# Performance work log

Hardware: AMD Instinct MI355X
Metric: run time of the kernel (lower is better)

Reference implementation:

```python
import jax, jax.numpy as jnp
import numpy as np


def setup_inputs() -> dict:
    key = jax.random.key(0)
    ks = jax.random.split(key, 15)
    B, r, d, h, na = 64, 64, 2048, 64, 256
    x = jax.random.normal(ks[0], (B, d, na), dtype=jnp.float32)
    L = jax.random.randint(ks[1], (B, 2, na), 0, 2).astype(jnp.float32)
    p = lambda i, shp: jax.random.normal(ks[i], shp, dtype=jnp.float32)
    return {
        "x": x, "L": L,
        "Aq": p(2, (r, d)), "Ak": p(3, (r, d)), "Av": p(4, (r, d)),
        "Aq1": p(5, (r, r)), "Ak1": p(6, (r, r)), "Av1": p(7, (r, r)),
        "Aq5": p(8, (r, r)), "Ak5": p(9, (r, r)), "Av5": p(10, (r, r)),
        "Ao": p(11, (r, r)), "Ao1": p(12, (r, r)), "Ao5": p(13, (h, r)),
    }


def reference(x, L, Aq, Ak, Av, Aq1, Ak1, Av1, Aq5, Ak5, Av5, Ao, Ao1, Ao5):
    B, d, na = x.shape
    # numNeighbors: count of L[:,0,:] >= 1 per batch, +1 -> [B,1,1]
    numN = jnp.sum((L[:, 0, :] >= 1.0).astype(jnp.float32), axis=1)[:, None, None] + 1.0
    scale = jnp.sqrt(numN)  # [B,1,1]

    def attn(M, Wq, Wk, Wv):
        # M: [B, f, na]; Wq/Wk/Wv: [r, f]
        Q = jax.nn.sigmoid(jnp.einsum('rf,bfn->bnr', Wq, M))  # [B,na,r]
        K = jax.nn.sigmoid(jnp.einsum('rf,bfn->brn', Wk, M))  # [B,r,na]
        V = jax.nn.sigmoid(jnp.einsum('rf,bfn->bnr', Wv, M))  # [B,na,r]
        A = jax.nn.softmax(jnp.einsum('bnr,brm->bnm', Q, K) / scale, axis=2)
        return jnp.einsum('bnm,bmr->brn', A, V)  # [B,r,na]

    o = attn(x, Aq, Ak, Av)
    M = jax.nn.silu(jnp.einsum('sr,brn->bsn', Ao, o))
    o = attn(M, Aq1, Ak1, Av1)
    M = jax.nn.silu(jnp.einsum('sr,brn->bsn', Ao1, o))
    o = attn(M, Aq5, Ak5, Av5)
    M = jax.nn.silu(jnp.einsum('hr,brn->bhn', Ao5, o))  # [B,h,na]

    blk = d // na  # rows per block (8)
    def diagvec(i):
        # kron(sum-of-squares, ones(1,2)) == repeat each element twice -> [B, 2*na]
        return jnp.repeat(jnp.sum(M[:, i * blk:(i + 1) * blk, :] ** 2, axis=1), 2, axis=1)

    M11, M12, M21, M22 = diagvec(0), diagvec(1), diagvec(2), diagvec(3)
    Mpp = jnp.sum(M[:, 4 * blk:, :] ** 2, axis=1)  # [B, na]

    # q = x[:, :4, :].transpose(1,2).reshape(B, 4*na) (agent-major ordering)
    q = jnp.transpose(x[:, :4, :], (0, 2, 1)).reshape(B, 4 * na)
    q1, q2 = q[:, :2 * na], q[:, 2 * na:]
    # Block matrix [[diag(M11), diag(M12)], [diag(M21), diag(M22)]] quadratic form,
    # computed without materializing the [B, 4na, 4na] matrix.
    quad = jnp.sum(M11 * q1 * q1 + M12 * q1 * q2 + M21 * q2 * q1 + M22 * q2 * q2,
                   axis=1, keepdims=True)
    return quad + jnp.sum(Mpp, axis=1, keepdims=True)  # [B, 1]
```

## Files before the change

### kernel.cpp

```cpp
#include <hip/hip_runtime.h>
#include <stdint.h>

typedef _Float16 f16;
typedef f16 f16x8 __attribute__((ext_vector_type(8)));
typedef float f32x4 __attribute__((ext_vector_type(4)));

#define MFMA(a,b,c) __builtin_amdgcn_mfma_f32_16x16x32_f16(a, b, c, 0, 0, 0)

__device__ __forceinline__ float sigmoidf_(float z) {
  return __builtin_amdgcn_rcpf(1.0f + __expf(-z));
}

__global__ void prep_kernel(const float* __restrict__ L,
    const float* __restrict__ Aq, const float* __restrict__ Ak, const float* __restrict__ Av,
    const float* __restrict__ Aq1, const float* __restrict__ Ak1, const float* __restrict__ Av1,
    const float* __restrict__ Aq5, const float* __restrict__ Ak5, const float* __restrict__ Av5,
    const float* __restrict__ Ao, const float* __restrict__ Ao1, const float* __restrict__ Ao5,
    float* __restrict__ scale, f16* __restrict__ Wcat, f16* __restrict__ Wsm,
    float* __restrict__ out)
{
  __shared__ float r4[4];
  int blk = blockIdx.x, t = threadIdx.x;
  if (blk < 64) {
    float v = (L[blk * 512 + t] >= 1.0f) ? 1.0f : 0.0f;
    #pragma unroll
    for (int off = 32; off; off >>= 1) v += __shfl_down(v, off);
    if ((t & 63) == 0) r4[t >> 6] = v;
    __syncthreads();
    if (t == 0) scale[blk] = sqrtf(r4[0] + r4[1] + r4[2] + r4[3] + 1.0f);
  } else if (blk < 160) {
    int base = (blk - 64) * 4096;
    for (int i = 0; i < 16; i++) {
      int idx = base + t + i * 256;
      int row = idx >> 11, col = idx & 2047;
      float v = (row < 64) ? Aq[row * 2048 + col]
              : (row < 128) ? Ak[(row - 64) * 2048 + col]
              : Av[(row - 128) * 2048 + col];
      Wcat[idx] = (f16)v;
    }
  } else if (blk < 169) {
    int j = blk - 160;
    const float* s = (j == 0) ? Aq1 : (j == 1) ? Ak1 : (j == 2) ? Av1 : (j == 3) ? Aq5
                   : (j == 4) ? Ak5 : (j == 5) ? Av5 : (j == 6) ? Ao : (j == 7) ? Ao1 : Ao5;
    for (int i = 0; i < 16; i++) { int idx = t + i * 256; Wsm[j * 4096 + idx] = (f16)s[idx]; }
  } else {
    if (t < 64) out[t] = 0.0f;
  }
}

__global__ __launch_bounds__(256) void qkv1_kernel(const float* __restrict__ x,
    const f16* __restrict__ Wcat, f16* __restrict__ Qt, f16* __restrict__ Kt,
    f16* __restrict__ Vg)
{
  int b = blockIdx.y, n0 = blockIdx.x * 32;
  int t = threadIdx.x, lane = t & 63, w = t >> 6;
  int l15 = lane & 15, q = lane >> 4;
  __shared__ f16 xt[2][32 * 76];
  __shared__ f16 wt[2][192 * 76];
  f32x4 acc[2][3] = {};
  const float* xb = x + (size_t)b * 524288 + n0;
  int tn = t & 31, fg = t >> 5;

  int r0 = t >> 3,           c0 = t & 7;
  int r1 = (t + 256) >> 3,   c1 = (t + 256) & 7;
  int r2 = (t + 512) >> 3,   c2 = (t + 512) & 7;
  int r3 = (t + 768) >> 3,   c3 = (t + 768) & 7;
  int r4 = (t + 1024) >> 3,  c4 = (t + 1024) & 7;
  int r5 = (t + 1280) >> 3,  c5 = (t + 1280) & 7;
  const f16* pw0 = Wcat + (size_t)r0 * 2048 + c0 * 8;
  const f16* pw1 = Wcat + (size_t)r1 * 2048 + c1 * 8;
  const f16* pw2 = Wcat + (size_t)r2 * 2048 + c2 * 8;
  const f16* pw3 = Wcat + (size_t)r3 * 2048 + c3 * 8;
  const f16* pw4 = Wcat + (size_t)r4 * 2048 + c4 * 8;
  const f16* pw5 = Wcat + (size_t)r5 * 2048 + c5 * 8;
  const float* px = xb + (size_t)(fg * 8) * 256 + tn;

  float xa0, xa1, xa2, xa3, xa4, xa5, xa6, xa7;
  uint4 wr0, wr1, wr2, wr3, wr4, wr5;

#define LOAD_X(f0n) do {                                                        \
    const float* xp_ = px + (size_t)(f0n) * 256;                                \
    xa0 = xp_[0];    xa1 = xp_[256];  xa2 = xp_[512];  xa3 = xp_[768];          \
    xa4 = xp_[1024]; xa5 = xp_[1280]; xa6 = xp_[1536]; xa7 = xp_[1792];         \
  } while (0)

#define LOAD_W(f0n) do {                                                        \
    wr0 = *(const uint4*)(pw0 + (f0n)); wr1 = *(const uint4*)(pw1 + (f0n));     \
    wr2 = *(const uint4*)(pw2 + (f0n)); wr3 = *(const uint4*)(pw3 + (f0n));     \
    wr4 = *(const uint4*)(pw4 + (f0n)); wr5 = *(const uint4*)(pw5 + (f0n));     \
  } while (0)

#define WRITE_XW(buf) do {                                                      \
    f16x8 pk_;                                                                  \
    pk_[0] = (f16)xa0; pk_[1] = (f16)xa1; pk_[2] = (f16)xa2; pk_[3] = (f16)xa3; \
    pk_[4] = (f16)xa4; pk_[5] = (f16)xa5; pk_[6] = (f16)xa6; pk_[7] = (f16)xa7; \
    *(f16x8*)&xt[buf][tn * 76 + fg * 8] = pk_;                                  \
    f16* wb_ = &wt[buf][0];                                                     \
    *(uint4*)&wb_[r0 * 76 + c0 * 8] = wr0;                                      \
    *(uint4*)&wb_[r1 * 76 + c1 * 8] = wr1;                                      \
    *(uint4*)&wb_[r2 * 76 + c2 * 8] = wr2;                                      \
    *(uint4*)&wb_[r3 * 76 + c3 * 8] = wr3;                                      \
    *(uint4*)&wb_[r4 * 76 + c4 * 8] = wr4;                                      \
    *(uint4*)&wb_[r5 * 76 + c5 * 8] = wr5;                                      \
  } while (0)

  LOAD_X(0);
  LOAD_W(0);
  WRITE_XW(0);
  __syncthreads();

  int cur = 0;
  for (int f0 = 0; f0 < 2048; f0 += 64) {
    int nxt = cur ^ 1;
    bool more = (f0 + 64 < 2048);
    if (more) { LOAD_X(f0 + 64); LOAD_W(f0 + 64); }

    #pragma unroll
    for (int ks = 0; ks < 2; ks++) {
      int k0 = ks * 32 + q * 8;
      f16x8 af[2], bf[3];
      af[0] = *(const f16x8*)&xt[cur][l15 * 76 + k0];
      af[1] = *(const f16x8*)&xt[cur][(16 + l15) * 76 + k0];
      #pragma unroll
      for (int j = 0; j < 3; j++) bf[j] = *(const f16x8*)&wt[cur][((w * 3 + j) * 16 + l15) * 76 + k0];
      #pragma unroll
      for (int nt = 0; nt < 2; nt++)
        #pragma unroll
        for (int j = 0; j < 3; j++)
          acc[nt][j] = MFMA(af[nt], bf[j], acc[nt][j]);
    }

    if (more) WRITE_XW(nxt);
    __syncthreads();
    cur = nxt;
  }
#undef LOAD_X
#undef LOAD_W
#undef WRITE_XW

  #pragma unroll
  for (int nt = 0; nt < 2; nt++)
    #pragma unroll
    for (int j = 0; j < 3; j++) {
      int rr = (w * 3 + j) * 16 + l15;
      float s[4];
      #pragma unroll
      for (int reg = 0; reg < 4; reg++) s[reg] = sigmoidf_(acc[nt][j][reg]);
      int nbase = n0 + nt * 16 + q * 4;
      if (rr < 64) {
        #pragma unroll
        for (int reg = 0; reg < 4; reg++)
          Qt[(size_t)b * 16384 + (size_t)(nbase + reg) * 64 + rr] = (f16)s[reg];
      } else if (rr < 128) {
        #pragma unroll
        for (int reg = 0; reg < 4; reg++)
          Kt[(size_t)b * 16384 + (size_t)(nbase + reg) * 64 + (rr - 64)] = (f16)s[reg];
      } else {
        union { f16 h[4]; uint2 u; } pk;
        #pragma unroll
        for (int reg = 0; reg < 4; reg++) pk.h[reg] = (f16)s[reg];
        *(uint2*)(Vg + (size_t)b * 16384 + (size_t)(rr - 128) * 256 + nbase) = pk.u;
      }
    }
}

template<int LAYER>
__global__ __launch_bounds__(1024) void attnB_kernel(const float* __restrict__ x,
    const float* __restrict__ scale, const f16* __restrict__ Wsm,
    const f16* __restrict__ Qtg, const f16* __restrict__ Ktg, const f16* __restrict__ Vgg,
    const f16* __restrict__ Min, f16* __restrict__ Mout, float* __restrict__ out)
{
  int g = blockIdx.x, b = blockIdx.y, n0 = g * 64;
  int t = threadIdx.x, lane = t & 63, w = t >> 6;
  int l15 = lane & 15, q = lane >> 4;
  __shared__ f16 KT[256 * 76];
  __shared__ f16 SM[256 * 76];
  __shared__ f16 VM[64 * 268];
  __shared__ f16 QT[64 * 76];
  __shared__ f16 OT[64 * 76];
  __shared__ float denomS[64];

  float sinv = __builtin_amdgcn_rcpf(scale[b]);
  if (t < 64) denomS[t] = 0.0f;

  const f16* Wq = Wsm + (size_t)(LAYER == 1 ? 0 : 3) * 4096;
  const f16* Wk = Wsm + (size_t)(LAYER == 1 ? 1 : 4) * 4096;
  const f16* Wv = Wsm + (size_t)(LAYER == 1 ? 2 : 5) * 4096;
  const f16* Wo = Wsm + (size_t)(LAYER == 0 ? 6 : (LAYER == 1 ? 7 : 8)) * 4096;

  f16x8 bkav[4][2];
  f16x8 wqa, wqb;
  if (LAYER > 0) {
    const f16* Wrole = (w < 8) ? Wk : Wv;
    #pragma unroll
    for (int rt = 0; rt < 4; rt++) {
      bkav[rt][0] = *(const f16x8*)(Wrole + (rt * 16 + l15) * 64 + q * 8);
      bkav[rt][1] = *(const f16x8*)(Wrole + (rt * 16 + l15) * 64 + 32 + q * 8);
    }
    int rtq = w & 3;
    wqa = *(const f16x8*)(Wq + (rtq * 16 + l15) * 64 + q * 8);
    wqb = *(const f16x8*)(Wq + (rtq * 16 + l15) * 64 + 32 + q * 8);
  }

  if (LAYER == 0) {
    if (t < 512) {
      const uint4* qs = (const uint4*)(Qtg + (size_t)b * 16384 + (size_t)n0 * 64);
      int n = t >> 3, c = t & 7; *(uint4*)&QT[n * 76 + c * 8] = qs[t];
    }
    const uint4* ks = (const uint4*)(Ktg + (size_t)b * 16384);
    const uint4* vs = (const uint4*)(Vgg + (size_t)b * 16384);
    #pragma unroll
    for (int i = 0; i < 2; i++) {
      int id = t + i * 1024;
      int m = id >> 3, c = id & 7;
      *(uint4*)&KT[m * 76 + c * 8] = ks[id];
      int r = id >> 5, c2 = id & 31;
      *(uint4*)&VM[r * 268 + c2 * 8] = vs[id];
    }
  } else {
    const uint4* ms = (const uint4*)(Min + (size_t)b * 16384);
    #pragma unroll
    for (int i = 0; i < 2; i++) {
      int id = t + i * 1024, m = id >> 3, c = id & 7;
      *(uint4*)&SM[m * 76 + c * 8] = ms[id];
    }
  }
  __syncthreads();

  if (LAYER > 0) {
    if (w < 8) {
      #pragma unroll
      for (int mi = 0; mi < 2; mi++) {
        int mt = w * 2 + mi;
        f16x8 a0 = *(const f16x8*)&SM[(mt * 16 + l15) * 76 + q * 8];
        f16x8 a1 = *(const f16x8*)&SM[(mt * 16 + l15) * 76 + 32 + q * 8];
        #pragma unroll
        for (int rt = 0; rt < 4; rt++) {
          f32x4 acc = {}; acc = MFMA(a0, bkav[rt][0], acc); acc = MFMA(a1, bkav[rt][1], acc);
          #pragma unroll
          for (int reg = 0; reg < 4; reg++)
            KT[(mt * 16 + q * 4 + reg) * 76 + rt * 16 + l15] = (f16)sigmoidf_(acc[reg]);
        }
      }
    } else {
      #pragma unroll
      for (int mi = 0; mi < 2; mi++) {
        int mt = (w - 8) * 2 + mi;
        f16x8 b0 = *(const f16x8*)&SM[(mt * 16 + l15) * 76 + q * 8];
        f16x8 b1 = *(const f16x8*)&SM[(mt * 16 + l15) * 76 + 32 + q * 8];
        #pragma unroll
        for (int rt = 0; rt < 4; rt++) {
          f32x4 acc = {}; acc = MFMA(bkav[rt][0], b0, acc); acc = MFMA(bkav[rt][1], b1, acc);
          #pragma unroll
          for (int reg = 0; reg < 4; reg++)
            VM[(rt * 16 + q * 4 + reg) * 268 + mt * 16 + l15] = (f16)sigmoidf_(acc[reg]);
        }
      }
    }
    {
      int nt = w >> 2, rt = w & 3;
      f16x8 a0 = *(const f16x8*)&SM[(n0 + nt * 16 + l15) * 76 + q * 8];
      f16x8 a1 = *(const f16x8*)&SM[(n0 + nt * 16 + l15) * 76 + 32 + q * 8];
      f32x4 acc = {}; acc = MFMA(a0, wqa, acc); acc = MFMA(a1, wqb, acc);
      #pragma unroll
      for (int reg = 0; reg < 4; reg++)
        QT[(nt * 16 + q * 4 + reg) * 76 + rt * 16 + l15] = (f16)sigmoidf_(acc[reg]);
    }
    __syncthreads();
  }

  {
    int nt = w >> 2;
    f16x8 a0 = *(const f16x8*)&QT[(nt * 16 + l15) * 76 + q * 8];
    f16x8 a1 = *(const f16x8*)&QT[(nt * 16 + l15) * 76 + 32 + q * 8];
    float dsum[4] = {0.f, 0.f, 0.f, 0.f};
    #pragma unroll
    for (int mi = 0; mi < 4; mi++) {
      int mt = (w & 3) * 4 + mi;
      f16x8 b0 = *(const f16x8*)&KT[(mt * 16 + l15) * 76 + q * 8];
      f16x8 b1 = *(const f16x8*)&KT[(mt * 16 + l15) * 76 + 32 + q * 8];
      f32x4 acc = {}; acc = MFMA(a0, b0, acc); acc = MFMA(a1, b1, acc);
      #pragma unroll
      for (int reg = 0; reg < 4; reg++) {
        float e = __expf(acc[reg] * sinv);
        dsum[reg] += e;
        SM[(nt * 16 + q * 4 + reg) * 268 + mt * 16 + l15] = (f16)e;
      }
    }
    #pragma unroll
    for (int reg = 0; reg < 4; reg++) {
      #pragma unroll
      for (int mask = 1; mask < 16; mask <<= 1) dsum[reg] += __shfl_xor(dsum[reg], mask);
    }
    if (l15 == 0) {
      #pragma unroll
      for (int reg = 0; reg < 4; reg++) atomicAdd(&denomS[nt * 16 + q * 4 + reg], dsum[reg]);
    }
  }
  __syncthreads();

  {
    int nt = w >> 2, rt = w & 3;
    f32x4 oacc = {};
    #pragma unroll
    for (int kc = 0; kc < 8; kc++) {
      f16x8 af = *(const f16x8*)&SM[(nt * 16 + l15) * 268 + kc * 32 + q * 8];
      f16x8 bf = *(const f16x8*)&VM[(rt * 16 + l15) * 268 + kc * 32 + q * 8];
      oacc = MFMA(af, bf, oacc);
    }
    float rden[4];
    #pragma unroll
    for (int reg = 0; reg < 4; reg++)
      rden[reg] = __builtin_amdgcn_rcpf(denomS[nt * 16 + q * 4 + reg]);
    #pragma unroll
    for (int reg = 0; reg < 4; reg++) {
      int row = nt * 16 + q * 4 + reg;
      OT[row * 76 + rt * 16 + l15] = (f16)(oacc[reg] * rden[reg]);
    }
  }
  __syncthreads();

  f16* Mst = QT;
  {
    int nt = w >> 2, st = w & 3;
    f16x8 a0 = *(const f16x8*)&OT[(nt * 16 + l15) * 76 + q * 8];
    f16x8 a1 = *(const f16x8*)&OT[(nt * 16 + l15) * 76 + 32 + q * 8];
    f16x8 b0 = *(const f16x8*)(Wo + (st * 16 + l15) * 64 + q * 8);
    f16x8 b1 = *(const f16x8*)(Wo + (st * 16 + l15) * 64 + 32 + q * 8);
    f32x4 acc = {}; acc = MFMA(a0, b0, acc); acc = MFMA(a1, b1, acc);
    #pragma unroll
    for (int reg = 0; reg < 4; reg++) {
      float z = acc[reg];
      Mst[(nt * 16 + q * 4 + reg) * 68 + st * 16 + l15] = (f16)(z * sigmoidf_(z));
    }
  }
  __syncthreads();

  if (LAYER < 2) {
    if (t < 512) {
      int row = t >> 3, c = t & 7;
      *(uint4*)(Mout + (size_t)b * 16384 + (size_t)(n0 + row) * 64 + c * 8)
          = *(const uint4*)&Mst[row * 68 + c * 8];
    }
  } else {
    float contrib = 0.0f;
    if (t < 64) {
      int ntok = n0 + t;
      const f16* row = &Mst[t * 68];
      float d[4] = {0, 0, 0, 0}, pp = 0.0f;
      #pragma unroll
      for (int gg = 0; gg < 8; gg++) {
        f16x8 v = *(const f16x8*)(row + gg * 8);
        float ss = 0.0f;
        #pragma unroll
        for (int k = 0; k < 8; k++) { float f = (float)v[k]; ss += f * f; }
        if (gg < 4) d[gg] = ss; else pp += ss;
      }
      int np = ntok >> 1, c0 = (ntok & 1) * 2;
      const float* xb = x + (size_t)b * 524288 + (size_t)c0 * 256;
      float q1a = xb[np], q1b = xb[256 + np];
      float q2a = xb[128 + np], q2b = xb[384 + np];
      contrib = d[0] * (q1a * q1a + q1b * q1b)
              + (d[1] + d[2]) * (q1a * q2a + q1b * q2b)
              + d[3] * (q2a * q2a + q2b * q2b) + pp;
    }
    if (w == 0) {
      #pragma unroll
      for (int off = 32; off; off >>= 1) contrib += __shfl_down(contrib, off);
      if (lane == 0) atomicAdd(out + b, contrib);
    }
  }
}

extern "C" void kernel_launch(void* const* d_in, const int* in_sizes, int n_in,
                              void* d_out, int out_size, void* d_ws, size_t ws_size,
                              hipStream_t stream) {
  const float* x   = (const float*)d_in[0];
  const float* L   = (const float*)d_in[1];
  const float* Aq  = (const float*)d_in[2];
  const float* Ak  = (const float*)d_in[3];
  const float* Av  = (const float*)d_in[4];
  const float* Aq1 = (const float*)d_in[5];
  const float* Ak1 = (const float*)d_in[6];
  const float* Av1 = (const float*)d_in[7];
  const float* Aq5 = (const float*)d_in[8];
  const float* Ak5 = (const float*)d_in[9];
  const float* Av5 = (const float*)d_in[10];
  const float* Ao  = (const float*)d_in[11];
  const float* Ao1 = (const float*)d_in[12];
  const float* Ao5 = (const float*)d_in[13];

  char* ws = (char*)d_ws;
  float* scale = (float*)ws;
  f16* Wcat  = (f16*)(ws + 256);
  f16* Wsm   = (f16*)(ws + 786688);
  f16* Qtg   = (f16*)(ws + 860416);
  f16* Ktg   = (f16*)(ws + 2957568);
  f16* Vgg   = (f16*)(ws + 5054720);
  f16* MbufA = (f16*)(ws + 7151872);
  f16* MbufB = (f16*)(ws + 9249024);
  float* out = (float*)d_out;

  prep_kernel<<<170, 256, 0, stream>>>(L, Aq, Ak, Av, Aq1, Ak1, Av1,
                                       Aq5, Ak5, Av5, Ao, Ao1, Ao5, scale, Wcat, Wsm, out);
  qkv1_kernel<<<dim3(8, 64), 256, 0, stream>>>(x, Wcat, Qtg, Ktg, Vgg);
  attnB_kernel<0><<<dim3(4, 64), 1024, 0, stream>>>(x, scale, Wsm, Qtg, Ktg, Vgg,
                                                    nullptr, MbufA, out);
  attnB_kernel<1><<<dim3(4, 64), 1024, 0, stream>>>(x, scale, Wsm, Qtg, Ktg, Vgg,
                                                    MbufA, MbufB, out);
  attnB_kernel<2><<<dim3(4, 64), 1024, 0, stream>>>(x, scale, Wsm, Qtg, Ktg, Vgg,
                                                    MbufB, nullptr, out);
}
```

Measured before the change: 268.2 us.

## Fuse three attention layers into one persistent kernel with grid barriers

Merges the three per-layer attention launches into a single kernel that loops over layers and synchronises all 256 blocks through an atomic-counter grid barrier. The scale computation and the small-weight fp16 conversion move into that kernel, which shrinks the prep kernel. The QKV projection kernel is retiled to 64 tokens by 128 features with 512 threads. The aim is to cut launch overhead and inter-kernel gaps. The grid barrier assumes all 256 blocks of 1024 threads are co-resident, which risks deadlock if they are not, and the spin-wait adds its own cost.

Measured after the change: 337.4 us. 1.26x slower.

```diff
diff --git a/kernel.cpp b/kernel.cpp
--- a/kernel.cpp
+++ b/kernel.cpp
@@ -11,25 +11,35 @@
   return __builtin_amdgcn_rcpf(1.0f + __expf(-z));
 }
 
-__global__ void prep_kernel(const float* __restrict__ L,
-    const float* __restrict__ Aq, const float* __restrict__ Ak, const float* __restrict__ Av,
-    const float* __restrict__ Aq1, const float* __restrict__ Ak1, const float* __restrict__ Av1,
-    const float* __restrict__ Aq5, const float* __restrict__ Ak5, const float* __restrict__ Av5,
-    const float* __restrict__ Ao, const float* __restrict__ Ao1, const float* __restrict__ Ao5,
-    float* __restrict__ scale, f16* __restrict__ Wcat, f16* __restrict__ Wsm,
-    float* __restrict__ out)
+__device__ __forceinline__ f16x8 ldw8(const float* __restrict__ p) {
+  union { uint4 u; float f[4]; } a, bqq;
+  a.u  = *(const uint4*)p;
+  bqq.u = *(const uint4*)(p + 4);
+  f16x8 r;
+  r[0] = (f16)a.f[0];  r[1] = (f16)a.f[1];  r[2] = (f16)a.f[2];  r[3] = (f16)a.f[3];
+  r[4] = (f16)bqq.f[0]; r[5] = (f16)bqq.f[1]; r[6] = (f16)bqq.f[2]; r[7] = (f16)bqq.f[3];
+  return r;
+}
+
+__device__ __forceinline__ void grid_bar(uint32_t* bar, uint32_t target) {
+  __syncthreads();
+  if (threadIdx.x == 0) {
+    __threadfence();
+    atomicAdd(bar, 1u);
+    while (__hip_atomic_load(bar, __ATOMIC_ACQUIRE, __HIP_MEMORY_SCOPE_AGENT) < target)
+      __builtin_amdgcn_s_sleep(2);
+    __threadfence();
+  }
+  __syncthreads();
+}
+
+__global__ void prep_kernel(const float* __restrict__ Aq, const float* __restrict__ Ak,
+                            const float* __restrict__ Av, f16* __restrict__ Wcat,
+                            uint32_t* __restrict__ bar, float* __restrict__ out)
 {
-  __shared__ float r4[4];
   int blk = blockIdx.x, t = threadIdx.x;
-  if (blk < 64) {
-    float v = (L[blk * 512 + t] >= 1.0f) ? 1.0f : 0.0f;
-    #pragma unroll
-    for (int off = 32; off; off >>= 1) v += __shfl_down(v, off);
-    if ((t & 63) == 0) r4[t >> 6] = v;
-    __syncthreads();
-    if (t == 0) scale[blk] = sqrtf(r4[0] + r4[1] + r4[2] + r4[3] + 1.0f);
-  } else if (blk < 160) {
-    int base = (blk - 64) * 4096;
+  if (blk < 96) {
+    int base = blk * 4096;
     for (int i = 0; i < 16; i++) {
       int idx = base + t + i * 256;
       int row = idx >> 11, col = idx & 2047;
@@ -38,91 +48,91 @@
               : Av[(row - 128) * 2048 + col];
       Wcat[idx] = (f16)v;
     }
-  } else if (blk < 169) {
-    int j = blk - 160;
-    const float* s = (j == 0) ? Aq1 : (j == 1) ? Ak1 : (j == 2) ? Av1 : (j == 3) ? Aq5
-                   : (j == 4) ? Ak5 : (j == 5) ? Av5 : (j == 6) ? Ao : (j == 7) ? Ao1 : Ao5;
-    for (int i = 0; i < 16; i++) { int idx = t + i * 256; Wsm[j * 4096 + idx] = (f16)s[idx]; }
   } else {
     if (t < 64) out[t] = 0.0f;
-  }
-}
-
-__global__ __launch_bounds__(256) void qkv1_kernel(const float* __restrict__ x,
+    if (t == 64) *bar = 0u;
+  }
+}
+
+__global__ __launch_bounds__(512) void qkv1_kernel(const float* __restrict__ x,
     const f16* __restrict__ Wcat, f16* __restrict__ Qt, f16* __restrict__ Kt,
     f16* __restrict__ Vg)
 {
-  int b = blockIdx.y, n0 = blockIdx.x * 32;
+  int b = blockIdx.y, n0 = blockIdx.x * 64;
   int t = threadIdx.x, lane = t & 63, w = t >> 6;
   int l15 = lane & 15, q = lane >> 4;
-  __shared__ f16 xt[2][32 * 76];
-  __shared__ f16 wt[2][192 * 76];
+  int nh = w >> 2, wr_ = w & 3;
+  __shared__ f16 xt[2][64 * 132];
+  __shared__ f16 wt[2][192 * 132];
   f32x4 acc[2][3] = {};
   const float* xb = x + (size_t)b * 524288 + n0;
-  int tn = t & 31, fg = t >> 5;
-
-  int r0 = t >> 3,           c0 = t & 7;
-  int r1 = (t + 256) >> 3,   c1 = (t + 256) & 7;
-  int r2 = (t + 512) >> 3,   c2 = (t + 512) & 7;
-  int r3 = (t + 768) >> 3,   c3 = (t + 768) & 7;
-  int r4 = (t + 1024) >> 3,  c4 = (t + 1024) & 7;
-  int r5 = (t + 1280) >> 3,  c5 = (t + 1280) & 7;
+  int tn = lane;
+  const float* px = xb + (size_t)(w * 16) * 256 + tn;
+
+  int r0 = t >> 4,           c0 = t & 15;
+  int r1 = (t + 512) >> 4,   c1 = (t + 512) & 15;
+  int r2 = (t + 1024) >> 4,  c2 = (t + 1024) & 15;
+  int r3 = (t + 1536) >> 4,  c3 = (t + 1536) & 15;
+  int r4 = (t + 2048) >> 4,  c4 = (t + 2048) & 15;
+  int r5 = (t + 2560) >> 4,  c5 = (t + 2560) & 15;
   const f16* pw0 = Wcat + (size_t)r0 * 2048 + c0 * 8;
   const f16* pw1 = Wcat + (size_t)r1 * 2048 + c1 * 8;
   const f16* pw2 = Wcat + (size_t)r2 * 2048 + c2 * 8;
   const f16* pw3 = Wcat + (size_t)r3 * 2048 + c3 * 8;
   const f16* pw4 = Wcat + (size_t)r4 * 2048 + c4 * 8;
   const f16* pw5 = Wcat + (size_t)r5 * 2048 + c5 * 8;
-  const float* px = xb + (size_t)(fg * 8) * 256 + tn;
 
   float xa0, xa1, xa2, xa3, xa4, xa5, xa6, xa7;
-  uint4 wr0, wr1, wr2, wr3, wr4, wr5;
-
-#define LOAD_X(f0n) do {                                                        \
-    const float* xp_ = px + (size_t)(f0n) * 256;                                \
-    xa0 = xp_[0];    xa1 = xp_[256];  xa2 = xp_[512];  xa3 = xp_[768];          \
-    xa4 = xp_[1024]; xa5 = xp_[1280]; xa6 = xp_[1536]; xa7 = xp_[1792];         \
+  float xa8, xa9, xa10, xa11, xa12, xa13, xa14, xa15;
+  uint4 wv0, wv1, wv2, wv3, wv4, wv5;
+
+#define LOAD_XW(f0n) do {                                                       \
+    const float* p_ = px + (size_t)(f0n) * 256;                                 \
+    xa0  = p_[0];    xa1  = p_[256];  xa2  = p_[512];  xa3  = p_[768];          \
+    xa4  = p_[1024]; xa5  = p_[1280]; xa6  = p_[1536]; xa7  = p_[1792];         \
+    xa8  = p_[2048]; xa9  = p_[2304]; xa10 = p_[2560]; xa11 = p_[2816];         \
+    xa12 = p_[3072]; xa13 = p_[3328]; xa14 = p_[3584]; xa15 = p_[3840];         \
+    wv0 = *(const uint4*)(pw0 + (f0n)); wv1 = *(const uint4*)(pw1 + (f0n));     \
+    wv2 = *(const uint4*)(pw2 + (f0n)); wv3 = *(const uint4*)(pw3 + (f0n));     \
+    wv4 = *(const uint4*)(pw4 + (f0n)); wv5 = *(const uint4*)(pw5 + (f0n));     \
   } while (0)
 
-#define LOAD_W(f0n) do {                                                        \
-    wr0 = *(const uint4*)(pw0 + (f0n)); wr1 = *(const uint4*)(pw1 + (f0n));     \
-    wr2 = *(const uint4*)(pw2 + (f0n)); wr3 = *(const uint4*)(pw3 + (f0n));     \
-    wr4 = *(const uint4*)(pw4 + (f0n)); wr5 = *(const uint4*)(pw5 + (f0n));     \
+#define WRITE_XW(buf) do {                                                      \
+    f16x8 pa_, pb_;                                                             \
+    pa_[0] = (f16)xa0;  pa_[1] = (f16)xa1;  pa_[2] = (f16)xa2;  pa_[3] = (f16)xa3;  \
+    pa_[4] = (f16)xa4;  pa_[5] = (f16)xa5;  pa_[6] = (f16)xa6;  pa_[7] = (f16)xa7;  \
+    pb_[0] = (f16)xa8;  pb_[1] = (f16)xa9;  pb_[2] = (f16)xa10; pb_[3] = (f16)xa11; \
+    pb_[4] = (f16)xa12; pb_[5] = (f16)xa13; pb_[6] = (f16)xa14; pb_[7] = (f16)xa15; \
+    *(f16x8*)&xt[buf][tn * 132 + w * 16]     = pa_;                             \
+    *(f16x8*)&xt[buf][tn * 132 + w * 16 + 8] = pb_;                             \
+    f16* wb_ = &wt[buf][0];                                                     \
+    *(uint4*)&wb_[r0 * 132 + c0 * 8] = wv0;                                     \
+    *(uint4*)&wb_[r1 * 132 + c1 * 8] = wv1;                                     \
+    *(uint4*)&wb_[r2 * 132 + c2 * 8] = wv2;                                     \
+    *(uint4*)&wb_[r3 * 132 + c3 * 8] = wv3;                                     \
+    *(uint4*)&wb_[r4 * 132 + c4 * 8] = wv4;                                     \
+    *(uint4*)&wb_[r5 * 132 + c5 * 8] = wv5;                                     \
   } while (0)
 
-#define WRITE_XW(buf) do {                                                      \
-    f16x8 pk_;                                                                  \
-    pk_[0] = (f16)xa0; pk_[1] = (f16)xa1; pk_[2] = (f16)xa2; pk_[3] = (f16)xa3; \
-    pk_[4] = (f16)xa4; pk_[5] = (f16)xa5; pk_[6] = (f16)xa6; pk_[7] = (f16)xa7; \
-    *(f16x8*)&xt[buf][tn * 76 + fg * 8] = pk_;                                  \
-    f16* wb_ = &wt[buf][0];                                                     \
-    *(uint4*)&wb_[r0 * 76 + c0 * 8] = wr0;                                      \
-    *(uint4*)&wb_[r1 * 76 + c1 * 8] = wr1;                                      \
-    *(uint4*)&wb_[r2 * 76 + c2 * 8] = wr2;                                      \
-    *(uint4*)&wb_[r3 * 76 + c3 * 8] = wr3;                                      \
-    *(uint4*)&wb_[r4 * 76 + c4 * 8] = wr4;                                      \
-    *(uint4*)&wb_[r5 * 76 + c5 * 8] = wr5;                                      \
-  } while (0)
-
-  LOAD_X(0);
-  LOAD_W(0);
+  LOAD_XW(0);
   WRITE_XW(0);
   __syncthreads();
 
   int cur = 0;
-  for (int f0 = 0; f0 < 2048; f0 += 64) {
+  for (int f0 = 0; f0 < 2048; f0 += 128) {
     int nxt = cur ^ 1;
-    bool more = (f0 + 64 < 2048);
-    if (more) { LOAD_X(f0 + 64); LOAD_W(f0 + 64); }
+    bool more = (f0 + 128 < 2048);
+    if (more) LOAD_XW(f0 + 128);
 
     #pragma unroll
-    for (int ks = 0; ks < 2; ks++) {
+    for (int ks = 0; ks < 4; ks++) {
       int k0 = ks * 32 + q * 8;
       f16x8 af[2], bf[3];
-      af[0] = *(const f16x8*)&xt[cur][l15 * 76 + k0];
-      af[1] = *(const f16x8*)&xt[cur][(16 + l15) * 76 + k0];
-      #pragma unroll
-      for (int j = 0; j < 3; j++) bf[j] = *(const f16x8*)&wt[cur][((w * 3 + j) * 16 + l15) * 76 + k0];
+      af[0] = *(const f16x8*)&xt[cur][(nh * 32 + l15) * 132 + k0];
+      af[1] = *(const f16x8*)&xt[cur][(nh * 32 + 16 + l15) * 132 + k0];
+      #pragma unroll
+      for (int j = 0; j < 3; j++)
+        bf[j] = *(const f16x8*)&wt[cur][((wr_ * 3 + j) * 16 + l15) * 132 + k0];
       #pragma unroll
       for (int nt = 0; nt < 2; nt++)
         #pragma unroll
@@ -134,19 +144,18 @@
     __syncthreads();
     cur = nxt;
   }
-#undef LOAD_X
-#undef LOAD_W
+#undef LOAD_XW
 #undef WRITE_XW
 
   #pragma unroll
   for (int nt = 0; nt < 2; nt++)
     #pragma unroll
     for (int j = 0; j < 3; j++) {
-      int rr = (w * 3 + j) * 16 + l15;
+      int rr = (wr_ * 3 + j) * 16 + l15;
       float s[4];
       #pragma unroll
       for (int reg = 0; reg < 4; reg++) s[reg] = sigmoidf_(acc[nt][j][reg]);
-      int nbase = n0 + nt * 16 + q * 4;
+      int nbase = n0 + nh * 32 + nt * 16 + q * 4;
       if (rr < 64) {
         #pragma unroll
         for (int reg = 0; reg < 4; reg++)
@@ -164,11 +173,14 @@
     }
 }
 
-template<int LAYER>
-__global__ __launch_bounds__(1024) void attnB_kernel(const float* __restrict__ x,
-    const float* __restrict__ scale, const f16* __restrict__ Wsm,
+__global__ __launch_bounds__(1024) void attn_fused_kernel(const float* __restrict__ x,
+    const float* __restrict__ L,
+    const float* __restrict__ Aq1, const float* __restrict__ Ak1, const float* __restrict__ Av1,
+    const float* __restrict__ Aq5, const float* __restrict__ Ak5, const float* __restrict__ Av5,
+    const float* __restrict__ Ao, const float* __restrict__ Ao1, const float* __restrict__ Ao5,
     const f16* __restrict__ Qtg, const f16* __restrict__ Ktg, const f16* __restrict__ Vgg,
-    const f16* __restrict__ Min, f16* __restrict__ Mout, float* __restrict__ out)
+    f16* __restrict__ MbufA, f16* __restrict__ MbufB,
+    uint32_t* __restrict__ bar, float* __restrict__ out)
 {
   int g = blockIdx.x, b = blockIdx.y, n0 = g * 64;
   int t = threadIdx.x, lane = t & 63, w = t >> 6;
@@ -179,195 +191,216 @@
   __shared__ f16 QT[64 * 76];
   __shared__ f16 OT[64 * 76];
   __shared__ float denomS[64];
-
-  float sinv = __builtin_amdgcn_rcpf(scale[b]);
-  if (t < 64) denomS[t] = 0.0f;
-
-  const f16* Wq = Wsm + (size_t)(LAYER == 1 ? 0 : 3) * 4096;
-  const f16* Wk = Wsm + (size_t)(LAYER == 1 ? 1 : 4) * 4096;
-  const f16* Wv = Wsm + (size_t)(LAYER == 1 ? 2 : 5) * 4096;
-  const f16* Wo = Wsm + (size_t)(LAYER == 0 ? 6 : (LAYER == 1 ? 7 : 8)) * 4096;
-
-  f16x8 bkav[4][2];
-  f16x8 wqa, wqb;
-  if (LAYER > 0) {
-    const f16* Wrole = (w < 8) ? Wk : Wv;
-    #pragma unroll
-    for (int rt = 0; rt < 4; rt++) {
-      bkav[rt][0] = *(const f16x8*)(Wrole + (rt * 16 + l15) * 64 + q * 8);
-      bkav[rt][1] = *(const f16x8*)(Wrole + (rt * 16 + l15) * 64 + 32 + q * 8);
-    }
-    int rtq = w & 3;
-    wqa = *(const f16x8*)(Wq + (rtq * 16 + l15) * 64 + q * 8);
-    wqb = *(const f16x8*)(Wq + (rtq * 16 + l15) * 64 + 32 + q * 8);
-  }
-
-  if (LAYER == 0) {
-    if (t < 512) {
-      const uint4* qs = (const uint4*)(Qtg + (size_t)b * 16384 + (size_t)n0 * 64);
-      int n = t >> 3, c = t & 7; *(uint4*)&QT[n * 76 + c * 8] = qs[t];
-    }
-    const uint4* ks = (const uint4*)(Ktg + (size_t)b * 16384);
-    const uint4* vs = (const uint4*)(Vgg + (size_t)b * 16384);
-    #pragma unroll
-    for (int i = 0; i < 2; i++) {
-      int id = t + i * 1024;
-      int m = id >> 3, c = id & 7;
-      *(uint4*)&KT[m * 76 + c * 8] = ks[id];
-      int r = id >> 5, c2 = id & 31;
-      *(uint4*)&VM[r * 268 + c2 * 8] = vs[id];
-    }
-  } else {
-    const uint4* ms = (const uint4*)(Min + (size_t)b * 16384);
-    #pragma unroll
-    for (int i = 0; i < 2; i++) {
-      int id = t + i * 1024, m = id >> 3, c = id & 7;
-      *(uint4*)&SM[m * 76 + c * 8] = ms[id];
-    }
-  }
+  __shared__ float scpart[9];
+
+  float sv = 0.0f;
+  if (t < 512) sv = (L[(size_t)b * 512 + t] >= 1.0f) ? 1.0f : 0.0f;
+  #pragma unroll
+  for (int off = 32; off; off >>= 1) sv += __shfl_down(sv, off);
+  if (w < 8 && lane == 0) scpart[w] = sv;
   __syncthreads();
-
-  if (LAYER > 0) {
-    if (w < 8) {
-      #pragma unroll
-      for (int mi = 0; mi < 2; mi++) {
-        int mt = w * 2 + mi;
-        f16x8 a0 = *(const f16x8*)&SM[(mt * 16 + l15) * 76 + q * 8];
-        f16x8 a1 = *(const f16x8*)&SM[(mt * 16 + l15) * 76 + 32 + q * 8];
-        #pragma unroll
-        for (int rt = 0; rt < 4; rt++) {
-          f32x4 acc = {}; acc = MFMA(a0, bkav[rt][0], acc); acc = MFMA(a1, bkav[rt][1], acc);
+  if (t == 0) {
+    float s = scpart[0] + scpart[1] + scpart[2] + scpart[3]
+            + scpart[4] + scpart[5] + scpart[6] + scpart[7];
+    scpart[8] = __builtin_amdgcn_rcpf(sqrtf(s + 1.0f));
+  }
+  __syncthreads();
+  float sinv = scpart[8];
+
+  float q1a = 0.f, q1b = 0.f, q2a = 0.f, q2b = 0.f;
+  if (t < 64) {
+    int ntok = n0 + t, np = ntok >> 1, c0e = (ntok & 1) * 2;
+    const float* xbq = x + (size_t)b * 524288 + (size_t)c0e * 256;
+    q1a = xbq[np]; q1b = xbq[256 + np]; q2a = xbq[128 + np]; q2b = xbq[384 + np];
+  }
+
+  f16x8 bkav[4][2], wqa, wqb;
+
+  for (int l = 0; l < 3; ++l) {
+    const float* Wqf = (l == 1) ? Aq1 : Aq5;
+    const float* Wkf = (l == 1) ? Ak1 : Ak5;
+    const float* Wvf = (l == 1) ? Av1 : Av5;
+    const float* Wof = (l == 0) ? Ao : (l == 1) ? Ao1 : Ao5;
+    const f16* Min = (l == 1) ? MbufA : MbufB;
+    f16* Mout = (l == 0) ? MbufA : MbufB;
+
+    if (t < 64) denomS[t] = 0.0f;
+
+    if (l > 0) {
+      const float* Wrole = (w < 8) ? Wkf : Wvf;
+      #pragma unroll
+      for (int rt = 0; rt < 4; rt++) {
+        bkav[rt][0] = ldw8(Wrole + (rt * 16 + l15) * 64 + q * 8);
+        bkav[rt][1] = ldw8(Wrole + (rt * 16 + l15) * 64 + 32 + q * 8);
+      }
+      int rtq = w & 3;
+      wqa = ldw8(Wqf + (rtq * 16 + l15) * 64 + q * 8);
+      wqb = ldw8(Wqf + (rtq * 16 + l15) * 64 + 32 + q * 8);
+    }
+
+    if (l == 0) {
+      if (t < 512) {
+        const uint4* qs = (const uint4*)(Qtg + (size_t)b * 16384 + (size_t)n0 * 64);
+        int n = t >> 3, c = t & 7; *(uint4*)&QT[n * 76 + c * 8] = qs[t];
+      }
+      const uint4* ks = (const uint4*)(Ktg + (size_t)b * 16384);
+      const uint4* vs = (const uint4*)(Vgg + (size_t)b * 16384);
+      #pragma unroll
+      for (int i = 0; i < 2; i++) {
+        int id = t + i * 1024;
+        int m = id >> 3, c = id & 7;
+        *(uint4*)&KT[m * 76 + c * 8] = ks[id];
+        int r = id >> 5, c2 = id & 31;
+        *(uint4*)&VM[r * 268 + c2 * 8] = vs[id];
+      }
+    } else {
+      const uint4* ms = (const uint4*)(Min + (size_t)b * 16384);
+      #pragma unroll
+      for (int i = 0; i < 2; i++) {
+        int id = t + i * 1024, m = id >> 3, c = id & 7;
+        *(uint4*)&SM[m * 76 + c * 8] = ms[id];
+      }
+    }
+    __syncthreads();
+
+    if (l > 0) {
+      if (w < 8) {
+        #pragma unroll
+        for (int mi = 0; mi < 2; mi++) {
+          int mt = w * 2 + mi;
+          f16x8 a0 = *(const f16x8*)&SM[(mt * 16 + l15) * 76 + q * 8];
+          f16x8 a1 = *(const f16x8*)&SM[(mt * 16 + l15) * 76 + 32 + q * 8];
           #pragma unroll
-          for (int reg = 0; reg < 4; reg++)
-            KT[(mt * 16 + q * 4 + reg) * 76 + rt * 16 + l15] = (f16)sigmoidf_(acc[reg]);
+          for (int rt = 0; rt < 4; rt++) {
+            f32x4 acc = {}; acc = MFMA(a0, bkav[rt][0], acc); acc = MFMA(a1, bkav[rt][1], acc);
+            #pragma unroll
+            for (int reg = 0; reg < 4; reg++)
+              KT[(mt * 16 + q * 4 + reg) * 76 + rt * 16 + l15] = (f16)sigmoidf_(acc[reg]);
+          }
         }
-      }
-    } else {
-      #pragma unroll
-      for (int mi = 0; mi < 2; mi++) {
-        int mt = (w - 8) * 2 + mi;
-        f16x8 b0 = *(const f16x8*)&SM[(mt * 16 + l15) * 76 + q * 8];
-        f16x8 b1 = *(const f16x8*)&SM[(mt * 16 + l15) * 76 + 32 + q * 8];
-        #pragma unroll
-        for (int rt = 0; rt < 4; rt++) {
-          f32x4 acc = {}; acc = MFMA(bkav[rt][0], b0, acc); acc = MFMA(bkav[rt][1], b1, acc);
+      } else {
+        #pragma unroll
+        for (int mi = 0; mi < 2; mi++) {
+          int mt = (w - 8) * 2 + mi;
+          f16x8 b0 = *(const f16x8*)&SM[(mt * 16 + l15) * 76 + q * 8];
+          f16x8 b1 = *(const f16x8*)&SM[(mt * 16 + l15) * 76 + 32 + q * 8];
           #pragma unroll
-          for (int reg = 0; reg < 4; reg++)
-            VM[(rt * 16 + q * 4 + reg) * 268 + mt * 16 + l15] = (f16)sigmoidf_(acc[reg]);
+          for (int rt = 0; rt < 4; rt++) {
+            f32x4 acc = {}; acc = MFMA(bkav[rt][0], b0, acc); acc = MFMA(bkav[rt][1], b1, acc);
+            #pragma unroll
+            for (int reg = 0; reg < 4; reg++)
+              VM[(rt * 16 + q * 4 + reg) * 268 + mt * 16 + l15] = (f16)sigmoidf_(acc[reg]);
+          }
         }
       }
-    }
+      {
+        int nt = w >> 2, rt = w & 3;
+        f16x8 a0 = *(const f16x8*)&SM[(n0 + nt * 16 + l15) * 76 + q * 8];
+        f16x8 a1 = *(const f16x8*)&SM[(n0 + nt * 16 + l15) * 76 + 32 + q * 8];
+        f32x4 acc = {}; acc = MFMA(a0, wqa, acc); acc = MFMA(a1, wqb, acc);
+        #pragma unroll
+        for (int reg = 0; reg < 4; reg++)
+          QT[(nt * 16 + q * 4 + reg) * 76 + rt * 16 + l15] = (f16)sigmoidf_(acc[reg]);
+      }
+      __syncthreads();
+    }
+
+    {
+      int nt = w >> 2;
+      f16x8 a0 = *(const f16x8*)&QT[(nt * 16 + l15) * 76 + q * 8];
+      f16x8 a1 = *(const f16x8*)&QT[(nt * 16 + l15) * 76 + 32 + q * 8];
+      float dsum[4] = {0.f, 0.f, 0.f, 0.f};
+      #pragma unroll
+      for (int mi = 0; mi < 4; mi++) {
+        int mt = (w & 3) * 4 + mi;
+        f16x8 b0 = *(const f16x8*)&KT[(mt * 16 + l15) * 76 + q * 8];
+        f16x8 b1 = *(const f16x8*)&KT[(mt * 16 + l15) * 76 + 32 + q * 8];
+        f32x4 acc = {}; acc = MFMA(a0, b0, acc); acc = MFMA(a1, b1, acc);
+        #pragma unroll
+        for (int reg = 0; reg < 4; reg++) {
+          float e = __expf(acc[reg] * sinv);
+          dsum[reg] += e;
+          SM[(nt * 16 + q * 4 + reg) * 268 + mt * 16 + l15] = (f16)e;
+        }
+      }
+      #pragma unroll
+      for (int reg = 0; reg < 4; reg++) {
+        #pragma unroll
+        for (int mask = 1; mask < 16; mask <<= 1) dsum[reg] += __shfl_xor(dsum[reg], mask);
+      }
+      if (l15 == 0) {
+        #pragma unroll
+        for (int reg = 0; reg < 4; reg++) atomicAdd(&denomS[nt * 16 + q * 4 + reg], dsum[reg]);
+      }
+    }
+    __syncthreads();
+
     {
       int nt = w >> 2, rt = w & 3;
-      f16x8 a0 = *(const f16x8*)&SM[(n0 + nt * 16 + l15) * 76 + q * 8];
-      f16x8 a1 = *(const f16x8*)&SM[(n0 + nt * 16 + l15) * 76 + 32 + q * 8];
-      f32x4 acc = {}; acc = MFMA(a0, wqa, acc); acc = MFMA(a1, wqb, acc);
+      f32x4 oacc = {};
+      #pragma unroll
+      for (int kc = 0; kc < 8; kc++) {
+        f16x8 af = *(const f16x8*)&SM[(nt * 16 + l15) * 268 + kc * 32 + q * 8];
+        f16x8 bf = *(const f16x8*)&VM[(rt * 16 + l15) * 268 + kc * 32 + q * 8];
+        oacc = MFMA(af, bf, oacc);
+      }
+      float rden[4];
       #pragma unroll
       for (int reg = 0; reg < 4; reg++)
-        QT[(nt * 16 + q * 4 + reg) * 76 + rt * 16 + l15] = (f16)sigmoidf_(acc[reg]);
+        rden[reg] = __builtin_amdgcn_rcpf(denomS[nt * 16 + q * 4 + reg]);
+      #pragma unroll
+      for (int reg = 0; reg < 4; reg++) {
+        int row = nt * 16 + q * 4 + reg;
+        OT[row * 76 + rt * 16 + l15] = (f16)(oacc[reg] * rden[reg]);
+      }
     }
     __syncthreads();
-  }
-
-  {
-    int nt = w >> 2;
-    f16x8 a0 = *(const f16x8*)&QT[(nt * 16 + l15) * 76 + q * 8];
-    f16x8 a1 = *(const f16x8*)&QT[(nt * 16 + l15) * 76 + 32 + q * 8];
-    float dsum[4] = {0.f, 0.f, 0.f, 0.f};
-    #pragma unroll
-    for (int mi = 0; mi < 4; mi++) {
-      int mt = (w & 3) * 4 + mi;
-      f16x8 b0 = *(const f16x8*)&KT[(mt * 16 + l15) * 76 + q * 8];
-      f16x8 b1 = *(const f16x8*)&KT[(mt * 16 + l15) * 76 + 32 + q * 8];
+
+    f16* Mst = QT;
+    {
+      int nt = w >> 2, st = w & 3;
+      f16x8 a0 = *(const f16x8*)&OT[(nt * 16 + l15) * 76 + q * 8];
+      f16x8 a1 = *(const f16x8*)&OT[(nt * 16 + l15) * 76 + 32 + q * 8];
+      f16x8 b0 = ldw8(Wof + (st * 16 + l15) * 64 + q * 8);
+      f16x8 b1 = ldw8(Wof + (st * 16 + l15) * 64 + 32 + q * 8);
       f32x4 acc = {}; acc = MFMA(a0, b0, acc); acc = MFMA(a1, b1, acc);
       #pragma unroll
       for (int reg = 0; reg < 4; reg++) {
-        float e = __expf(acc[reg] * sinv);
-        dsum[reg] += e;
-        SM[(nt * 16 + q * 4 + reg) * 268 + mt * 16 + l15] = (f16)e;
-      }
-    }
-    #pragma unroll
-    for (int reg = 0; reg < 4; reg++) {
-      #pragma unroll
-      for (int mask = 1; mask < 16; mask <<= 1) dsum[reg] += __shfl_xor(dsum[reg], mask);
-    }
-    if (l15 == 0) {
-      #pragma unroll
-      for (int reg = 0; reg < 4; reg++) atomicAdd(&denomS[nt * 16 + q * 4 + reg], dsum[reg]);
-    }
-  }
-  __syncthreads();
-
-  {
-    int nt = w >> 2, rt = w & 3;
-    f32x4 oacc = {};
-    #pragma unroll
-    for (int kc = 0; kc < 8; kc++) {
-      f16x8 af = *(const f16x8*)&SM[(nt * 16 + l15) * 268 + kc * 32 + q * 8];
-      f16x8 bf = *(const f16x8*)&VM[(rt * 16 + l15) * 268 + kc * 32 + q * 8];
-      oacc = MFMA(af, bf, oacc);
-    }
-    float rden[4];
-    #pragma unroll
-    for (int reg = 0; reg < 4; reg++)
-      rden[reg] = __builtin_amdgcn_rcpf(denomS[nt * 16 + q * 4 + reg]);
-    #pragma unroll
-    for (int reg = 0; reg < 4; reg++) {
-      int row = nt * 16 + q * 4 + reg;
-      OT[row * 76 + rt * 16 + l15] = (f16)(oacc[reg] * rden[reg]);
-    }
-  }
-  __syncthreads();
-
-  f16* Mst = QT;
-  {
-    int nt = w >> 2, st = w & 3;
-    f16x8 a0 = *(const f16x8*)&OT[(nt * 16 + l15) * 76 + q * 8];
-    f16x8 a1 = *(const f16x8*)&OT[(nt * 16 + l15) * 76 + 32 + q * 8];
-    f16x8 b0 = *(const f16x8*)(Wo + (st * 16 + l15) * 64 + q * 8);
-    f16x8 b1 = *(const f16x8*)(Wo + (st * 16 + l15) * 64 + 32 + q * 8);
-    f32x4 acc = {}; acc = MFMA(a0, b0, acc); acc = MFMA(a1, b1, acc);
-    #pragma unroll
-    for (int reg = 0; reg < 4; reg++) {
-      float z = acc[reg];
-      Mst[(nt * 16 + q * 4 + reg) * 68 + st * 16 + l15] = (f16)(z * sigmoidf_(z));
-    }
-  }
-  __syncthreads();
-
-  if (LAYER < 2) {
-    if (t < 512) {
-      int row = t >> 3, c = t & 7;
-      *(uint4*)(Mout + (size_t)b * 16384 + (size_t)(n0 + row) * 64 + c * 8)
-          = *(const uint4*)&Mst[row * 68 + c * 8];
-    }
-  } else {
-    float contrib = 0.0f;
-    if (t < 64) {
-      int ntok = n0 + t;
-      const f16* row = &Mst[t * 68];
-      float d[4] = {0, 0, 0, 0}, pp = 0.0f;
-      #pragma unroll
-      for (int gg = 0; gg < 8; gg++) {
-        f16x8 v = *(const f16x8*)(row + gg * 8);
-        float ss = 0.0f;
-        #pragma unroll
-        for (int k = 0; k < 8; k++) { float f = (float)v[k]; ss += f * f; }
-        if (gg < 4) d[gg] = ss; else pp += ss;
-      }
-      int np = ntok >> 1, c0 = (ntok & 1) * 2;
-      const float* xb = x + (size_t)b * 524288 + (size_t)c0 * 256;
-      float q1a = xb[np], q1b = xb[256 + np];
-      float q2a = xb[128 + np], q2b = xb[384 + np];
-      contrib = d[0] * (q1a * q1a + q1b * q1b)
-              + (d[1] + d[2]) * (q1a * q2a + q1b * q2b)
-              + d[3] * (q2a * q2a + q2b * q2b) + pp;
-    }
-    if (w == 0) {
-      #pragma unroll
-      for (int off = 32; off; off >>= 1) contrib += __shfl_down(contrib, off);
-      if (lane == 0) atomicAdd(out + b, contrib);
+        float z = acc[reg];
+        Mst[(nt * 16 + q * 4 + reg) * 68 + st * 16 + l15] = (f16)(z * sigmoidf_(z));
+      }
+    }
+    __syncthreads();
+
+    if (l < 2) {
+      if (t < 512) {
+        int row = t >> 3, c = t & 7;
+        *(uint4*)(Mout + (size_t)b * 16384 + (size_t)(n0 + row) * 64 + c * 8)
+            = *(const uint4*)&Mst[row * 68 + c * 8];
+      }
+      grid_bar(bar, 256u * (uint32_t)(l + 1));
+    } else {
+      float contrib = 0.0f;
+      if (t < 64) {
+        const f16* row = &Mst[t * 68];
+        float d[4] = {0, 0, 0, 0}, pp = 0.0f;
+        #pragma unroll
+        for (int gg = 0; gg < 8; gg++) {
+          f16x8 v = *(const f16x8*)(row + gg * 8);
+          float ss = 0.0f;
+          #pragma unroll
+          for (int k = 0; k < 8; k++) { float f = (float)v[k]; ss += f * f; }
+          if (gg < 4) d[gg] = ss; else pp += ss;
+        }
+        contrib = d[0] * (q1a * q1a + q1b * q1b)
+                + (d[1] + d[2]) * (q1a * q2a + q1b * q2b)
+                + d[3] * (q2a * q2a + q2b * q2b) + pp;
+      }
+      if (w == 0) {
+        #pragma unroll
+        for (int off = 32; off; off >>= 1) contrib += __shfl_down(contrib, off);
+        if (lane == 0) atomicAdd(out + b, contrib);
+      }
     }
   }
 }
@@ -391,9 +424,8 @@
   const float* Ao5 = (const float*)d_in[13];
 
   char* ws = (char*)d_ws;
-  float* scale = (float*)ws;
+  uint32_t* bar = (uint32_t*)ws;
   f16* Wcat  = (f16*)(ws + 256);
-  f16* Wsm   = (f16*)(ws + 786688);
   f16* Qtg   = (f16*)(ws + 860416);
   f16* Ktg   = (f16*)(ws + 2957568);
   f16* Vgg   = (f16*)(ws + 5054720);
@@ -401,13 +433,9 @@
   f16* MbufB = (f16*)(ws + 9249024);
   float* out = (float*)d_out;
 
-  prep_kernel<<<170, 256, 0, stream>>>(L, Aq, Ak, Av, Aq1, Ak1, Av1,
-                                       Aq5, Ak5, Av5, Ao, Ao1, Ao5, scale, Wcat, Wsm, out);
-  qkv1_kernel<<<dim3(8, 64), 256, 0, stream>>>(x, Wcat, Qtg, Ktg, Vgg);
-  attnB_kernel<0><<<dim3(4, 64), 1024, 0, stream>>>(x, scale, Wsm, Qtg, Ktg, Vgg,
-                                                    nullptr, MbufA, out);
-  attnB_kernel<1><<<dim3(4, 64), 1024, 0, stream>>>(x, scale, Wsm, Qtg, Ktg, Vgg,
-                                                    MbufA, MbufB, out);
-  attnB_kernel<2><<<dim3(4, 64), 1024, 0, stream>>>(x, scale, Wsm, Qtg, Ktg, Vgg,
-                                                    MbufB, nullptr, out);
-}
+  prep_kernel<<<97, 256, 0, stream>>>(Aq, Ak, Av, Wcat, bar, out);
+  qkv1_kernel<<<dim3(4, 64), 512, 0, stream>>>(x, Wcat, Qtg, Ktg, Vgg);
+  attn_fused_kernel<<<dim3(4, 64), 1024, 0, stream>>>(x, L,
+      Aq1, Ak1, Av1, Aq5, Ak5, Av5, Ao, Ao1, Ao5,
+      Qtg, Ktg, Vgg, MbufA, MbufB, bar, out);
+}
```
